# Optimization experiments

Hardware: AMD Instinct MI355X
Metric: run time of the kernel (lower is better)

The kernel has to match this reference:

```python
import jax, jax.numpy as jnp
import numpy as np

B, N, DIM = 8, 1024, 1024
HEADS, DIM_HEAD = 16, 64
INNER = HEADS * DIM_HEAD  # 1024


def setup_inputs() -> dict:
    key = jax.random.key(0)
    k1, k2, k3 = jax.random.split(key, 3)
    x = jax.random.normal(k1, (B, N, DIM), dtype=jnp.float32)
    # Dense kernels (Glorot-ish scale for numerical sanity)
    w_qkv = jax.random.normal(k2, (DIM, 3 * INNER), dtype=jnp.float32) * (DIM ** -0.5)
    w_out = jax.random.normal(k3, (INNER, DIM), dtype=jnp.float32) * (INNER ** -0.5)
    b_out = jnp.zeros((DIM,), dtype=jnp.float32)
    return {"x": x, "w_qkv": w_qkv, "w_out": w_out, "b_out": b_out}


def reference(x, w_qkv, w_out, b_out):
    scale = DIM_HEAD ** -0.5
    qkv = x @ w_qkv                                   # [B, N, 3*INNER]
    q, k, v = jnp.split(qkv, 3, axis=-1)              # each [B, N, INNER]

    def to_heads(t):
        # [B, N, H*Dh] -> [B, H, N, Dh]
        return t.reshape(B, N, HEADS, DIM_HEAD).transpose(0, 2, 1, 3)

    q, k, v = to_heads(q), to_heads(k), to_heads(v)
    dots = jnp.einsum("bhid,bhjd->bhij", q, k) * scale   # [B, H, N, N]
    attn = jax.nn.softmax(dots, axis=-1)
    out = jnp.einsum("bhij,bhjd->bhid", attn, v)          # [B, H, N, Dh]
    out = out.transpose(0, 2, 1, 3).reshape(B, N, INNER)  # merge heads
    return out @ w_out + b_out                            # project_out (dropout inactive at inference)
```

## Files before the change

kernel.cpp:

```cpp
#include <hip/hip_runtime.h>
#include <hip/hip_bf16.h>
#include <math.h>

typedef __bf16 bf16_t;
typedef __bf16 bf16x4 __attribute__((ext_vector_type(4)));
typedef __bf16 bf16x8 __attribute__((ext_vector_type(8)));
typedef float f32x4 __attribute__((ext_vector_type(4)));

#define LOG2E 1.44269504088896340736f

#define GL2LDS(g, l)                                                     \
  __builtin_amdgcn_global_load_lds(                                      \
      (const __attribute__((address_space(1))) unsigned int*)(g),        \
      (__attribute__((address_space(3))) unsigned int*)(l), 16, 0, 0)

#define BAR() asm volatile("s_barrier" ::: "memory")
#define VMCNT(n) asm volatile("s_waitcnt vmcnt(" #n ")" ::: "memory")
#define LGKM0()                                         \
  do {                                                  \
    asm volatile("s_waitcnt lgkmcnt(0)" ::: "memory");  \
    __builtin_amdgcn_sched_barrier(0);                  \
  } while (0)

__global__ __launch_bounds__(256) void convert_f32_bf16(const float* __restrict__ in,
                                                        bf16_t* __restrict__ out) {
  const size_t idx = (size_t)(blockIdx.x * 256 + threadIdx.x) * 8;
  f32x4 a = *(const f32x4*)&in[idx];
  f32x4 b = *(const f32x4*)&in[idx + 4];
  bf16x8 v;
#pragma unroll
  for (int i = 0; i < 4; i++) { v[i] = (bf16_t)a[i]; v[i + 4] = (bf16_t)b[i]; }
  *(bf16x8*)&out[idx] = v;
}

__global__ __launch_bounds__(256) void transpose_f32_bf16(const float* __restrict__ in,
                                                          bf16_t* __restrict__ out,
                                                          int R, int C) {
  __shared__ bf16_t t[64][65];
  const int c0 = blockIdx.x * 64, r0 = blockIdx.y * 64;
  const int tx = threadIdx.x, ty = threadIdx.y;
#pragma unroll
  for (int i = 0; i < 16; i++) {
    int r = ty + i * 4;
    t[r][tx] = (bf16_t)in[(size_t)(r0 + r) * C + c0 + tx];
  }
  __syncthreads();
#pragma unroll
  for (int i = 0; i < 16; i++) {
    int r = ty + i * 4;
    out[(size_t)(c0 + r) * R + r0 + tx] = t[tx][r];
  }
}

template <int MODE>
__global__ __launch_bounds__(256, 4) void gemmT(const bf16_t* __restrict__ A,
                                                const bf16_t* __restrict__ Bt,
                                                bf16_t* __restrict__ Qb,
                                                bf16_t* __restrict__ Kb,
                                                bf16_t* __restrict__ Vtb,
                                                const float* __restrict__ bias,
                                                float* __restrict__ Out) {
  constexpr int K = 1024;
  constexpr int NT = K / 32;
  __shared__ __align__(16) bf16_t As[3][128 * 32];
  __shared__ __align__(16) bf16_t Bs[3][128 * 32];
  const int gx = gridDim.x;
  const int lin = blockIdx.y * gx + blockIdx.x;
  const int per = (gx * gridDim.y) >> 3;
  const int swz = (lin & 7) * per + (lin >> 3);
  const int m0 = (swz / gx) * 128, n0 = (swz % gx) * 128;
  const int tid = threadIdx.x;
  const int w = tid >> 6, l = tid & 63;
  const int lr = l & 15, lq = l >> 4;
  const int wm = w >> 1, wn = w & 1;

  const int rs = tid >> 2, ps = tid & 3;
  const int cs = (ps ^ ((rs >> 1) & 3)) * 8;
  const size_t gA0 = (size_t)(m0 + rs) * K + cs;
  const size_t gA1 = (size_t)(m0 + 64 + rs) * K + cs;
  const size_t gB0 = (size_t)(n0 + rs) * K + cs;
  const size_t gB1 = (size_t)(n0 + 64 + rs) * K + cs;
  const int ldsu0 = (w * 64) * 8;
  const int ldsu1 = (256 + w * 64) * 8;

#define STG(bf_, kt_)                                   \
  do {                                                  \
    const size_t kk_ = (size_t)(kt_) * 32;              \
    GL2LDS(&A[gA0 + kk_], &As[bf_][ldsu0]);             \
    GL2LDS(&A[gA1 + kk_], &As[bf_][ldsu1]);             \
    GL2LDS(&Bt[gB0 + kk_], &Bs[bf_][ldsu0]);            \
    GL2LDS(&Bt[gB1 + kk_], &Bs[bf_][ldsu1]);            \
  } while (0)

  int aoff[4], boff[4];
#pragma unroll
  for (int mf = 0; mf < 4; mf++) {
    const int row = wm * 64 + mf * 16 + lr;
    aoff[mf] = row * 32 + ((lq ^ ((row >> 1) & 3)) << 3);
  }
#pragma unroll
  for (int nf = 0; nf < 4; nf++) {
    const int row = wn * 64 + nf * 16 + lr;
    boff[nf] = row * 32 + ((lq ^ ((row >> 1) & 3)) << 3);
  }

  f32x4 acc[4][4] = {};

  STG(0, 0);
  STG(1, 1);
  VMCNT(4);
  BAR();

  for (int t = 0; t < NT; ++t) {
    const int bufR = t % 3;
    if (t + 2 < NT) STG((t + 2) % 3, t + 2);
    bf16x8 af[4], bv[4];
#pragma unroll
    for (int mf = 0; mf < 4; mf++)
      af[mf] = *(const bf16x8*)&As[bufR][aoff[mf]];
#pragma unroll
    for (int nf = 0; nf < 4; nf++)
      bv[nf] = *(const bf16x8*)&Bs[bufR][boff[nf]];
    LGKM0();
    __builtin_amdgcn_s_setprio(1);
#pragma unroll
    for (int mf = 0; mf < 4; mf++)
#pragma unroll
      for (int nf = 0; nf < 4; nf++)
        acc[mf][nf] = __builtin_amdgcn_mfma_f32_16x16x32_bf16(af[mf], bv[nf],
                                                              acc[mf][nf], 0, 0, 0);
    __builtin_amdgcn_s_setprio(0);
    if (t == NT - 2) { VMCNT(0); } else if (t < NT - 2) { VMCNT(4); }
    BAR();
  }

#pragma unroll
  for (int mf = 0; mf < 4; mf++)
#pragma unroll
    for (int nf = 0; nf < 4; nf++)
#pragma unroll
      for (int i = 0; i < 4; i++) {
        const int m = m0 + wm * 64 + mf * 16 + lq * 4 + i;
        const int c = n0 + wn * 64 + nf * 16 + lr;
        const float v = acc[mf][nf][i];
        if (MODE == 1) {
          Out[(size_t)m * 1024 + c] = v + bias[c];
        } else {
          const int b = m >> 10, n = m & 1023;
          const int which = c >> 10, cc = c & 1023;
          const int hh = cc >> 6, d = cc & 63;
          const size_t qk = ((size_t)((b * 16 + hh) * 1024 + n)) * 64 + d;
          if (which == 0)
            Qb[qk] = (bf16_t)(v * (0.125f * LOG2E));
          else if (which == 1)
            Kb[qk] = (bf16_t)v;
          else
            Vtb[((size_t)((b * 16 + hh) * 64 + d)) * 1024 + n] = (bf16_t)v;
        }
      }
}

#define PS  72
__global__ __launch_bounds__(256) void attn128(const bf16_t* __restrict__ Qb,
                                               const bf16_t* __restrict__ Kb,
                                               const bf16_t* __restrict__ Vtb,
                                               bf16_t* __restrict__ Ob) {
  __shared__ __align__(16) bf16_t Ks[2][64 * 64];
  __shared__ __align__(16) bf16_t Vs[2][64 * 64];
  __shared__ __align__(16) bf16_t Pl[4 * 32 * PS];
  const int bid = blockIdx.x;
  const int qt = bid >> 7, b = (bid >> 4) & 7, h = bid & 15;
  const bf16_t* Qh = Qb + (size_t)((b * 16 + h) * 1024) * 64;
  const bf16_t* Kh = Kb + (size_t)((b * 16 + h) * 1024) * 64;
  const bf16_t* Vh = Vtb + (size_t)((b * 16 + h) * 64) * 1024;
  const int tid = threadIdx.x, w = tid >> 6, l = tid & 63;
  const int lr = l & 15, lq = l >> 4;
  const int q0 = qt * 128 + w * 32;
  const int swz = (lr >> 1) & 3;
  const int g7 = (lr >> 1) & 7;
  const int kc0 = (lq ^ g7) * 8;
  const int kc1 = ((4 + lq) ^ g7) * 8;

  bf16x8 onesA;
#pragma unroll
  for (int i = 0; i < 8; i++) onesA[i] = (bf16_t)1.0f;

  const int r0 = tid >> 3, r1 = r0 + 32, p0 = tid & 7;
  const int ck0 = (p0 ^ ((r0 >> 1) & 7)) * 8;
  const int ck1 = (p0 ^ ((r1 >> 1) & 7)) * 8;
  const int ldsS0 = (w * 64) * 8;
  const int ldsS1 = (256 + w * 64) * 8;

#define STGKV(bf_, j_)                                                  \
  do {                                                                  \
    const size_t jb = (size_t)(j_) * 64;                                \
    GL2LDS(&Kh[(jb + r0) * 64 + ck0], &Ks[bf_][ldsS0]);                 \
    GL2LDS(&Kh[(jb + r1) * 64 + ck1], &Ks[bf_][ldsS1]);                 \
    GL2LDS(&Vh[(size_t)r0 * 1024 + jb + ck0], &Vs[bf_][ldsS0]);         \
    GL2LDS(&Vh[(size_t)r1 * 1024 + jb + ck1], &Vs[bf_][ldsS1]);         \
  } while (0)

  bf16x8 qf[2][2];
#pragma unroll
  for (int mf = 0; mf < 2; mf++)
#pragma unroll
    for (int ks = 0; ks < 2; ks++)
      qf[mf][ks] = *(const bf16x8*)&Qh[(size_t)(q0 + mf * 16 + lr) * 64 + ks * 32 + lq * 8];

  STGKV(0, 0);
  VMCNT(0);
  BAR();

  f32x4 o[4][2] = {};
  f32x4 o5[2] = {};
  bf16_t* pw = &Pl[w * 32 * PS];

  for (int it = 0; it < 16; ++it) {
    const int buf = it & 1;
    if (it < 15) STGKV(buf ^ 1, it + 1);
    f32x4 s[4][2] = {};
    __builtin_amdgcn_s_setprio(1);
#pragma unroll
    for (int ks = 0; ks < 2; ks++)
#pragma unroll
      for (int nf = 0; nf < 4; nf++) {
        bf16x8 kf = *(const bf16x8*)&Ks[buf][(nf * 16 + lr) * 64 + (ks ? kc1 : kc0)];
#pragma unroll
        for (int mf = 0; mf < 2; mf++)
          s[nf][mf] = __builtin_amdgcn_mfma_f32_16x16x32_bf16(kf, qf[mf][ks], s[nf][mf], 0, 0, 0);
      }
    __builtin_amdgcn_s_setprio(0);
#pragma unroll
    for (int mf = 0; mf < 2; mf++)
#pragma unroll
      for (int nf = 0; nf < 4; nf++) {
        bf16x4 pk;
#pragma unroll
        for (int i = 0; i < 4; i++) pk[i] = (bf16_t)exp2f(s[nf][mf][i]);
        *(bf16x4*)&pw[(mf * 16 + lr) * PS + (((nf * 2 + (lq >> 1)) ^ swz) << 3) +
                      (lq & 1) * 4] = pk;
      }
    __builtin_amdgcn_s_setprio(1);
#pragma unroll
    for (int ks = 0; ks < 2; ks++) {
      bf16x8 pf[2];
#pragma unroll
      for (int mf = 0; mf < 2; mf++)
        pf[mf] = *(const bf16x8*)&pw[(mf * 16 + lr) * PS + ((ks * 4 + (lq ^ swz)) << 3)];
#pragma unroll
      for (int df = 0; df < 4; df++) {
        bf16x8 vf = *(const bf16x8*)&Vs[buf][(df * 16 + lr) * 64 + (ks ? kc1 : kc0)];
#pragma unroll
        for (int mf = 0; mf < 2; mf++)
          o[df][mf] = __builtin_amdgcn_mfma_f32_16x16x32_bf16(vf, pf[mf], o[df][mf], 0, 0, 0);
      }
#pragma unroll
      for (int mf = 0; mf < 2; mf++)
        o5[mf] = __builtin_amdgcn_mfma_f32_16x16x32_bf16(onesA, pf[mf], o5[mf], 0, 0, 0);
    }
    __builtin_amdgcn_s_setprio(0);
    VMCNT(0);
    BAR();
  }
#pragma unroll
  for (int mf = 0; mf < 2; mf++) {
    const float inv = 1.0f / o5[mf][0];
    const int grow = b * 1024 + q0 + mf * 16 + lr;
#pragma unroll
    for (int df = 0; df < 4; df++) {
      bf16x4 ov;
#pragma unroll
      for (int i = 0; i < 4; i++) ov[i] = (bf16_t)(o[df][mf][i] * inv);
      *(bf16x4*)&Ob[(size_t)grow * 1024 + h * 64 + df * 16 + lq * 4] = ov;
    }
  }
}

extern "C" void kernel_launch(void* const* d_in, const int* in_sizes, int n_in,
                              void* d_out, int out_size, void* d_ws, size_t ws_size,
                              hipStream_t stream) {
  const float* x     = (const float*)d_in[0];
  const float* w_qkv = (const float*)d_in[1];
  const float* w_out = (const float*)d_in[2];
  const float* b_out = (const float*)d_in[3];
  float* out = (float*)d_out;

  bf16_t* ws = (bf16_t*)d_ws;
  const size_t SZ = (size_t)8 * 1024 * 1024;
  bf16_t* Qb  = ws;
  bf16_t* Kb  = Qb + SZ;
  bf16_t* Vtb = Kb + SZ;
  bf16_t* Ob  = Vtb + SZ;
  bf16_t* Wqt = Ob + SZ;
  bf16_t* Wot = Wqt + (size_t)3072 * 1024;
  bf16_t* Xb  = Ob;

  hipLaunchKernelGGL(convert_f32_bf16, dim3(4096), dim3(256), 0, stream, x, Xb);
  hipLaunchKernelGGL(transpose_f32_bf16, dim3(48, 16), dim3(64, 4), 0, stream,
                     w_qkv, Wqt, 1024, 3072);
  hipLaunchKernelGGL(transpose_f32_bf16, dim3(16, 16), dim3(64, 4), 0, stream,
                     w_out, Wot, 1024, 1024);
  hipLaunchKernelGGL((gemmT<0>), dim3(24, 64), dim3(256), 0, stream,
                     Xb, Wqt, Qb, Kb, Vtb, (const float*)nullptr, (float*)nullptr);
  hipLaunchKernelGGL(attn128, dim3(1024), dim3(256), 0, stream, Qb, Kb, Vtb, Ob);
  hipLaunchKernelGGL((gemmT<1>), dim3(8, 64), dim3(256), 0, stream,
                     Ob, Wot, (bf16_t*)nullptr, (bf16_t*)nullptr, (bf16_t*)nullptr,
                     b_out, out);
}
```

Before: 276.0 us.

## Switch attention to 32x32x16 MFMA with register-shuffled P and scalar denominators

Rewrites the attention inner loop to use 32x32x16 bf16 MFMAs instead of 16x16x32. The P tile now stays in registers and is passed to the PV MFMA through cross-half lane shuffles, replacing the LDS round-trip through the Pl buffer. The softmax denominator is summed in scalar registers instead of with an extra ones-matrix MFMA, and the K/V LDS swizzle is simplified to match the new access pattern. This removes LDS traffic and MFMA work, at the cost of more shuffle instructions and larger accumulator register use.

```diff
diff --git a/kernel.cpp b/kernel.cpp
--- a/kernel.cpp
+++ b/kernel.cpp
@@ -3,9 +3,11 @@
 #include <math.h>
 
 typedef __bf16 bf16_t;
+typedef __bf16 bf16x2 __attribute__((ext_vector_type(2)));
 typedef __bf16 bf16x4 __attribute__((ext_vector_type(4)));
 typedef __bf16 bf16x8 __attribute__((ext_vector_type(8)));
 typedef float f32x4 __attribute__((ext_vector_type(4)));
+typedef float f32x16 __attribute__((ext_vector_type(16)));
 
 #define LOG2E 1.44269504088896340736f
 
@@ -21,6 +23,13 @@
     asm volatile("s_waitcnt lgkmcnt(0)" ::: "memory");  \
     __builtin_amdgcn_sched_barrier(0);                  \
   } while (0)
+
+static __device__ __forceinline__ unsigned pk2(bf16_t a, bf16_t b) {
+  bf16x2 t;
+  t[0] = a;
+  t[1] = b;
+  return __builtin_bit_cast(unsigned, t);
+}
 
 __global__ __launch_bounds__(256) void convert_f32_bf16(const float* __restrict__ in,
                                                         bf16_t* __restrict__ out) {
@@ -160,120 +169,117 @@
       }
 }
 
-#define PS  72
 __global__ __launch_bounds__(256) void attn128(const bf16_t* __restrict__ Qb,
                                                const bf16_t* __restrict__ Kb,
                                                const bf16_t* __restrict__ Vtb,
                                                bf16_t* __restrict__ Ob) {
   __shared__ __align__(16) bf16_t Ks[2][64 * 64];
   __shared__ __align__(16) bf16_t Vs[2][64 * 64];
-  __shared__ __align__(16) bf16_t Pl[4 * 32 * PS];
   const int bid = blockIdx.x;
   const int qt = bid >> 7, b = (bid >> 4) & 7, h = bid & 15;
   const bf16_t* Qh = Qb + (size_t)((b * 16 + h) * 1024) * 64;
   const bf16_t* Kh = Kb + (size_t)((b * 16 + h) * 1024) * 64;
   const bf16_t* Vh = Vtb + (size_t)((b * 16 + h) * 64) * 1024;
   const int tid = threadIdx.x, w = tid >> 6, l = tid & 63;
-  const int lr = l & 15, lq = l >> 4;
-  const int q0 = qt * 128 + w * 32;
-  const int swz = (lr >> 1) & 3;
-  const int g7 = (lr >> 1) & 7;
-  const int kc0 = (lq ^ g7) * 8;
-  const int kc1 = ((4 + lq) ^ g7) * 8;
-
-  bf16x8 onesA;
-#pragma unroll
-  for (int i = 0; i < 8; i++) onesA[i] = (bf16_t)1.0f;
-
-  const int r0 = tid >> 3, r1 = r0 + 32, p0 = tid & 7;
-  const int ck0 = (p0 ^ ((r0 >> 1) & 7)) * 8;
-  const int ck1 = (p0 ^ ((r1 >> 1) & 7)) * 8;
+  const int lq31 = l & 31, hi = l >> 5;
+  const int q0w = qt * 128 + w * 32;
+  const int ksw = lq31 & 7;
+
+  const int r0 = tid >> 3, p0 = tid & 7;
+  const int ck = (p0 ^ (r0 & 7)) * 8;
   const int ldsS0 = (w * 64) * 8;
   const int ldsS1 = (256 + w * 64) * 8;
 
 #define STGKV(bf_, j_)                                                  \
   do {                                                                  \
     const size_t jb = (size_t)(j_) * 64;                                \
-    GL2LDS(&Kh[(jb + r0) * 64 + ck0], &Ks[bf_][ldsS0]);                 \
-    GL2LDS(&Kh[(jb + r1) * 64 + ck1], &Ks[bf_][ldsS1]);                 \
-    GL2LDS(&Vh[(size_t)r0 * 1024 + jb + ck0], &Vs[bf_][ldsS0]);         \
-    GL2LDS(&Vh[(size_t)r1 * 1024 + jb + ck1], &Vs[bf_][ldsS1]);         \
+    GL2LDS(&Kh[(jb + r0) * 64 + ck], &Ks[bf_][ldsS0]);                  \
+    GL2LDS(&Kh[(jb + r0 + 32) * 64 + ck], &Ks[bf_][ldsS1]);             \
+    GL2LDS(&Vh[(size_t)r0 * 1024 + jb + ck], &Vs[bf_][ldsS0]);          \
+    GL2LDS(&Vh[(size_t)(r0 + 32) * 1024 + jb + ck], &Vs[bf_][ldsS1]);   \
   } while (0)
 
-  bf16x8 qf[2][2];
-#pragma unroll
-  for (int mf = 0; mf < 2; mf++)
-#pragma unroll
-    for (int ks = 0; ks < 2; ks++)
-      qf[mf][ks] = *(const bf16x8*)&Qh[(size_t)(q0 + mf * 16 + lr) * 64 + ks * 32 + lq * 8];
+  bf16x8 qf[4];
+#pragma unroll
+  for (int c = 0; c < 4; c++)
+    qf[c] = *(const bf16x8*)&Qh[(size_t)(q0w + lq31) * 64 + c * 16 + hi * 8];
 
   STGKV(0, 0);
   VMCNT(0);
   BAR();
 
-  f32x4 o[4][2] = {};
-  f32x4 o5[2] = {};
-  bf16_t* pw = &Pl[w * 32 * PS];
+  f32x16 o0 = {}, o1 = {};
+  float denom = 0.0f;
 
   for (int it = 0; it < 16; ++it) {
     const int buf = it & 1;
     if (it < 15) STGKV(buf ^ 1, it + 1);
-    f32x4 s[4][2] = {};
+    f32x16 s0 = {}, s1 = {};
     __builtin_amdgcn_s_setprio(1);
 #pragma unroll
-    for (int ks = 0; ks < 2; ks++)
-#pragma unroll
-      for (int nf = 0; nf < 4; nf++) {
-        bf16x8 kf = *(const bf16x8*)&Ks[buf][(nf * 16 + lr) * 64 + (ks ? kc1 : kc0)];
-#pragma unroll
-        for (int mf = 0; mf < 2; mf++)
-          s[nf][mf] = __builtin_amdgcn_mfma_f32_16x16x32_bf16(kf, qf[mf][ks], s[nf][mf], 0, 0, 0);
-      }
+    for (int c = 0; c < 4; c++) {
+      const int col = ((c * 2 + hi) ^ ksw) << 3;
+      bf16x8 kf0 = *(const bf16x8*)&Ks[buf][lq31 * 64 + col];
+      bf16x8 kf1 = *(const bf16x8*)&Ks[buf][(32 + lq31) * 64 + col];
+      s0 = __builtin_amdgcn_mfma_f32_32x32x16_bf16(kf0, qf[c], s0, 0, 0, 0);
+      s1 = __builtin_amdgcn_mfma_f32_32x32x16_bf16(kf1, qf[c], s1, 0, 0, 0);
+    }
     __builtin_amdgcn_s_setprio(0);
-#pragma unroll
-    for (int mf = 0; mf < 2; mf++)
-#pragma unroll
-      for (int nf = 0; nf < 4; nf++) {
-        bf16x4 pk;
-#pragma unroll
-        for (int i = 0; i < 4; i++) pk[i] = (bf16_t)exp2f(s[nf][mf][i]);
-        *(bf16x4*)&pw[(mf * 16 + lr) * PS + (((nf * 2 + (lq >> 1)) ^ swz) << 3) +
-                      (lq & 1) * 4] = pk;
-      }
+    unsigned wds[16];
+    float dl = 0.0f;
+#pragma unroll
+    for (int j = 0; j < 8; j++) {
+      bf16_t e0 = (bf16_t)exp2f(s0[2 * j]), e1 = (bf16_t)exp2f(s0[2 * j + 1]);
+      dl += (float)e0 + (float)e1;
+      wds[j] = pk2(e0, e1);
+    }
+#pragma unroll
+    for (int j = 0; j < 8; j++) {
+      bf16_t e0 = (bf16_t)exp2f(s1[2 * j]), e1 = (bf16_t)exp2f(s1[2 * j + 1]);
+      dl += (float)e0 + (float)e1;
+      wds[8 + j] = pk2(e0, e1);
+    }
+    denom += dl + __shfl_xor(dl, 32);
+    bf16x8 pf[4];
+#pragma unroll
+    for (int q2 = 0; q2 < 4; q2++) {
+      const int base = (q2 >> 1) * 8 + (q2 & 1) * 4;
+      const unsigned a0 = wds[base], a1 = wds[base + 1];
+      const unsigned a2 = wds[base + 2], a3 = wds[base + 3];
+      const unsigned x0 = __shfl_xor(a0, 32), x1 = __shfl_xor(a1, 32);
+      const unsigned x2 = __shfl_xor(a2, 32), x3 = __shfl_xor(a3, 32);
+      union { unsigned u[4]; bf16x8 v; } u;
+      u.u[0] = hi ? x2 : a0;
+      u.u[1] = hi ? x3 : a1;
+      u.u[2] = hi ? a2 : x0;
+      u.u[3] = hi ? a3 : x1;
+      pf[q2] = u.v;
+    }
     __builtin_amdgcn_s_setprio(1);
 #pragma unroll
-    for (int ks = 0; ks < 2; ks++) {
-      bf16x8 pf[2];
-#pragma unroll
-      for (int mf = 0; mf < 2; mf++)
-        pf[mf] = *(const bf16x8*)&pw[(mf * 16 + lr) * PS + ((ks * 4 + (lq ^ swz)) << 3)];
-#pragma unroll
-      for (int df = 0; df < 4; df++) {
-        bf16x8 vf = *(const bf16x8*)&Vs[buf][(df * 16 + lr) * 64 + (ks ? kc1 : kc0)];
-#pragma unroll
-        for (int mf = 0; mf < 2; mf++)
-          o[df][mf] = __builtin_amdgcn_mfma_f32_16x16x32_bf16(vf, pf[mf], o[df][mf], 0, 0, 0);
-      }
-#pragma unroll
-      for (int mf = 0; mf < 2; mf++)
-        o5[mf] = __builtin_amdgcn_mfma_f32_16x16x32_bf16(onesA, pf[mf], o5[mf], 0, 0, 0);
+    for (int c = 0; c < 4; c++) {
+      const int col = ((c * 2 + hi) ^ ksw) << 3;
+      bf16x8 vf0 = *(const bf16x8*)&Vs[buf][lq31 * 64 + col];
+      bf16x8 vf1 = *(const bf16x8*)&Vs[buf][(32 + lq31) * 64 + col];
+      o0 = __builtin_amdgcn_mfma_f32_32x32x16_bf16(vf0, pf[c], o0, 0, 0, 0);
+      o1 = __builtin_amdgcn_mfma_f32_32x32x16_bf16(vf1, pf[c], o1, 0, 0, 0);
     }
     __builtin_amdgcn_s_setprio(0);
     VMCNT(0);
     BAR();
   }
-#pragma unroll
-  for (int mf = 0; mf < 2; mf++) {
-    const float inv = 1.0f / o5[mf][0];
-    const int grow = b * 1024 + q0 + mf * 16 + lr;
-#pragma unroll
-    for (int df = 0; df < 4; df++) {
+  const float inv = 1.0f / denom;
+  const int grow = b * 1024 + q0w + lq31;
+#pragma unroll
+  for (int db = 0; db < 2; db++)
+#pragma unroll
+    for (int rg = 0; rg < 4; rg++) {
       bf16x4 ov;
 #pragma unroll
-      for (int i = 0; i < 4; i++) ov[i] = (bf16_t)(o[df][mf][i] * inv);
-      *(bf16x4*)&Ob[(size_t)grow * 1024 + h * 64 + df * 16 + lq * 4] = ov;
-    }
-  }
+      for (int i = 0; i < 4; i++)
+        ov[i] = (bf16_t)((db ? o1[rg * 4 + i] : o0[rg * 4 + i]) * inv);
+      *(bf16x4*)&Ob[(size_t)grow * 1024 + h * 64 + db * 32 + rg * 8 + hi * 4] = ov;
+    }
 }
 
 extern "C" void kernel_launch(void* const* d_in, const int* in_sizes, int n_in,
```

Result: slower. 285.9 us (+3.6%).
